# Optimization experiments

Hardware: AMD Instinct MI355X
Metric: run time of the kernel (lower is better)

Reference implementation:

```python
import jax, jax.numpy as jnp
import numpy as np

H = 16      # query heads
KV = 4      # kv heads
HD = 128    # head dim
THETA = 10000.0
NEG = -1e9


def _rope_tables(S, dtype):
    inv_freq = 1.0 / (THETA ** (jnp.arange(0, HD, 2, dtype=jnp.float32) / HD))
    ang = jnp.arange(S, dtype=jnp.float32)[:, None] * inv_freq[None, :]  # [S, HD/2]
    emb = jnp.concatenate([ang, ang], axis=-1)  # [S, HD]
    return jnp.cos(emb).astype(dtype), jnp.sin(emb).astype(dtype)


def _rotate_half(x):
    x1, x2 = jnp.split(x, 2, axis=-1)
    return jnp.concatenate([-x2, x1], axis=-1)


def _apply_rope(t, cos, sin):
    # t: [B, h, S, HD]; cos/sin: [S, HD]
    return t * cos[None, None] + _rotate_half(t) * sin[None, None]


def setup_inputs() -> dict:
    key = jax.random.key(0)
    ks = jax.random.split(key, 5)
    B, S, D = 2, 2048, 2048
    sc = 0.02
    return {
        "x": jax.random.normal(ks[0], (B, S, D), jnp.float32),
        "wq": jax.random.normal(ks[1], (D, D), jnp.float32) * sc,
        "wk": jax.random.normal(ks[2], (KV * HD, D), jnp.float32) * sc,
        "wv": jax.random.normal(ks[3], (KV * HD, D), jnp.float32) * sc,
        "wo": jax.random.normal(ks[4], (D, D), jnp.float32) * sc,
    }


def reference(x, wq, wk, wv, wo):
    B, S, D = x.shape
    q = (x @ wq.T).reshape(B, S, H, HD).transpose(0, 2, 1, 3)   # [B,H,S,HD]
    k = (x @ wk.T).reshape(B, S, KV, HD).transpose(0, 2, 1, 3)  # [B,KV,S,HD]
    v = (x @ wv.T).reshape(B, S, KV, HD).transpose(0, 2, 1, 3)

    cos, sin = _rope_tables(S, x.dtype)
    q = _apply_rope(q, cos, sin)
    k = _apply_rope(k, cos, sin)

    # GQA: repeat kv heads to match query heads (q_group_num = H // KV)
    k = jnp.repeat(k, H // KV, axis=1)  # [B,H,S,HD]
    v = jnp.repeat(v, H // KV, axis=1)

    scores = jnp.einsum("bhqd,bhkd->bhqk", q, k) / jnp.sqrt(jnp.float32(HD)).astype(x.dtype)
    causal = jnp.where(jnp.tril(jnp.ones((S, S), bool)), 0.0, NEG).astype(jnp.float32)
    attn = jax.nn.softmax(scores.astype(jnp.float32) + causal, axis=-1).astype(x.dtype)

    out = jnp.einsum("bhqk,bhkd->bhqd", attn, v)  # [B,H,S,HD]
    out = out.transpose(0, 2, 1, 3).reshape(B, S, D)
    return out @ wo.T
```

## Files before the change

kernel.cpp:

```cpp
#include <hip/hip_runtime.h>
#include <math.h>

typedef unsigned short u16;
typedef __attribute__((ext_vector_type(8))) short short8;
typedef __attribute__((ext_vector_type(8))) __bf16 bf16x8;
typedef __attribute__((ext_vector_type(4))) float floatx4;
typedef __attribute__((ext_vector_type(16))) float floatx16;
typedef __attribute__((ext_vector_type(4))) unsigned short u16x4;
typedef __attribute__((ext_vector_type(4))) float float4v;
typedef __attribute__((ext_vector_type(4))) unsigned int uint4v;

static __device__ __forceinline__ float b2f(u16 u) {
  unsigned int x = ((unsigned int)u) << 16;
  return __builtin_bit_cast(float, x);
}
static __device__ __forceinline__ u16 f2b(float f) {
  unsigned int x = __builtin_bit_cast(unsigned int, f);
  x += 0x7fffu + ((x >> 16) & 1u);
  return (u16)(x >> 16);
}
static __device__ __forceinline__ unsigned int pk2(float lo, float hi) {
  unsigned int r;
  asm("v_cvt_pk_bf16_f32 %0, %1, %2" : "=v"(r) : "v"(lo), "v"(hi));
  return r;
}
static __device__ __forceinline__ void gload_lds16(const void* g, void* l) {
  __builtin_amdgcn_global_load_lds(
      (const __attribute__((address_space(1))) unsigned int*)g,
      (__attribute__((address_space(3))) unsigned int*)l, 16, 0, 0);
}

__global__ __launch_bounds__(256) void cvt5_kernel(
    const float* __restrict__ x, const float* __restrict__ wq,
    const float* __restrict__ wk, const float* __restrict__ wv,
    const float* __restrict__ wo, u16* __restrict__ xb, u16* __restrict__ wqb,
    u16* __restrict__ wkb, u16* __restrict__ wvb, u16* __restrict__ wob) {
  int bid = blockIdx.x;
  const float* in;
  u16* out;
  int i0;
  if (bid < 8192) { in = x; out = xb; i0 = bid; }
  else if (bid < 12288) { in = wq; out = wqb; i0 = bid - 8192; }
  else if (bid < 13312) { in = wk; out = wkb; i0 = bid - 12288; }
  else if (bid < 14336) { in = wv; out = wvb; i0 = bid - 13312; }
  else { in = wo; out = wob; i0 = bid - 14336; }
  int i = i0 * 256 + threadIdx.x;
  float4v v = reinterpret_cast<const float4v*>(in)[i];
  u16x4 o;
  o[0] = f2b(v[0]); o[1] = f2b(v[1]); o[2] = f2b(v[2]); o[3] = f2b(v[3]);
  reinterpret_cast<u16x4*>(out)[i] = o;
}

__global__ __launch_bounds__(256) void rope_table_kernel(float* __restrict__ ct,
                                                         float* __restrict__ st) {
  int idx = blockIdx.x * 256 + threadIdx.x;
  int s = idx >> 6, j = idx & 63;
  float inv = powf(10000.0f, -(float)j * (1.0f / 64.0f));
  float ang = (float)s * inv;
  ct[idx] = cosf(ang);
  st[idx] = sinf(ang);
}

__global__ __launch_bounds__(256) void rope_k_kernel(const u16* __restrict__ in,
                                                     u16* __restrict__ out,
                                                     const float* __restrict__ ct,
                                                     const float* __restrict__ st) {
  int idx = blockIdx.x * 256 + threadIdx.x;
  int jc = idx & 7;
  int rest = idx >> 3;
  int h = rest & 3;
  int bs = rest >> 2;
  int s = bs & 2047;
  int b = bs >> 11;
  int j0 = jc * 8;
  size_t inoff = (size_t)bs * 3072 + 2048 + h * 128 + j0;
  short8 lo = *reinterpret_cast<const short8*>(&in[inoff]);
  short8 hi = *reinterpret_cast<const short8*>(&in[inoff + 64]);
  short8 o0, o1;
#pragma unroll
  for (int e = 0; e < 8; ++e) {
    float c = ct[s * 64 + j0 + e], sn = st[s * 64 + j0 + e];
    float t1 = b2f((u16)lo[e]);
    float t2 = b2f((u16)hi[e]);
    o0[e] = (short)f2b(t1 * c - t2 * sn);
    o1[e] = (short)f2b(t2 * c + t1 * sn);
  }
  size_t ooff = ((size_t)(b * 4 + h) * 2048 + s) * 128 + j0;
  *reinterpret_cast<short8*>(&out[ooff]) = o0;
  *reinterpret_cast<short8*>(&out[ooff + 64]) = o1;
}

__global__ __launch_bounds__(256) void vtrans_kernel(const u16* __restrict__ in,
                                                     u16* __restrict__ out) {
  __shared__ u16 t[128][66];
  int s0 = blockIdx.x * 64;
  int b = blockIdx.y >> 2, kv = blockIdx.y & 3;
  int tid = threadIdx.x;
#pragma unroll
  for (int it = 0; it < 32; ++it) {
    int idx = it * 256 + tid;
    int sl = idx >> 7, d = idx & 127;
    t[d][sl] = in[(size_t)(b * 2048 + s0 + sl) * 3072 + 2560 + kv * 128 + d];
  }
  __syncthreads();
#pragma unroll
  for (int it = 0; it < 32; ++it) {
    int idx = it * 256 + tid;
    int d = idx >> 6, sl = idx & 63;
    out[(size_t)((b * 4 + kv) * 128 + d) * 2048 + s0 + sl] = t[d][sl];
  }
}

static __device__ __forceinline__ void store_out(u16* p, float v) { *p = f2b(v); }
static __device__ __forceinline__ void store_out(float* p, float v) { *p = v; }

template <typename OutT>
__global__ __launch_bounds__(256) void gemm_bt(const u16* __restrict__ A,
                                               const u16* __restrict__ B,
                                               OutT* __restrict__ C, int M, int N, int K) {
  __shared__ __align__(16) u16 Al[128 * 32];
  __shared__ __align__(16) u16 Bl[128 * 32];
  const int tid = threadIdx.x;
  const int lane = tid & 63;
  const int w = tid >> 6;
  const int wr = w >> 1, wc = w & 1;
  const int lr = lane & 15, lg = lane >> 4;
  const int brow = blockIdx.y, bcol = blockIdx.x;
  const int r0 = lane >> 2, kp = lane & 3;
  const u16* Ag = A + (size_t)(brow * 128) * K;
  const u16* Bg = B + (size_t)(bcol * 128) * K;
  floatx4 acc[4][4] = {};
  for (int k0 = 0; k0 < K; k0 += 32) {
#pragma unroll
    for (int j = 0; j < 2; ++j) {
      int c = w * 2 + j;
      int row = c * 16 + r0;
      gload_lds16(Ag + (size_t)row * K + k0 + kp * 8, &Al[c * 512]);
      gload_lds16(Bg + (size_t)row * K + k0 + kp * 8, &Bl[c * 512]);
    }
    __syncthreads();
    bf16x8 af[4], bfr[4];
#pragma unroll
    for (int m = 0; m < 4; ++m)
      af[m] = *reinterpret_cast<const bf16x8*>(&Al[(wr * 64 + m * 16 + lr) * 32 + lg * 8]);
#pragma unroll
    for (int n = 0; n < 4; ++n)
      bfr[n] = *reinterpret_cast<const bf16x8*>(&Bl[(wc * 64 + n * 16 + lr) * 32 + lg * 8]);
#pragma unroll
    for (int m = 0; m < 4; ++m)
#pragma unroll
      for (int n = 0; n < 4; ++n)
        acc[m][n] = __builtin_amdgcn_mfma_f32_16x16x32_bf16(af[m], bfr[n], acc[m][n], 0, 0, 0);
    __syncthreads();
  }
#pragma unroll
  for (int m = 0; m < 4; ++m) {
    int row = brow * 128 + wr * 64 + m * 16 + lg * 4;
#pragma unroll
    for (int n = 0; n < 4; ++n) {
      int col = bcol * 128 + wc * 64 + n * 16 + lr;
#pragma unroll
      for (int i = 0; i < 4; ++i) store_out(&C[(size_t)(row + i) * N + col], acc[m][n][i]);
    }
  }
}

__global__ __launch_bounds__(256, 2) void attn_kernel(
    const u16* __restrict__ QKV, const u16* __restrict__ K,
    const u16* __restrict__ V, const float* __restrict__ ct,
    const float* __restrict__ st, u16* __restrict__ O, u16* __restrict__ Opart,
    float* __restrict__ Mpart, float* __restrict__ Lpart) {
  __shared__ __align__(16) u16 Kl[2][64 * 128];
  __shared__ __align__(16) u16 Vl[2][128 * 64];
  const int tid = threadIdx.x, lane = tid & 63, w = tid >> 6;
  const int ql = lane & 31, h2 = lane >> 5;
  const int idx = blockIdx.x;
  const int bh = idx & 31, pp = (idx >> 5) & 7, half = idx >> 8;
  const int b = bh >> 4, hh = bh & 15, kv = hh >> 2;
  const int t_l = 15 - pp, t_s = pp;
  const int pidx = bh * 8 + pp;
  const u16* Kp = K + (size_t)(b * 4 + kv) * 2048 * 128;
  const u16* Vp = V + (size_t)(b * 4 + kv) * 128 * 2048;
  const float cl = 0.08838834764831845f * 1.44269504088896f;

  auto stage = [&](int buf, int kb) {
#pragma unroll
    for (int j = 0; j < 4; ++j) {
      int slot = j * 256 + tid;
      int row = slot >> 4, d16 = slot & 15;
      gload_lds16(Kp + (size_t)(kb * 64 + row) * 128 + (d16 ^ (row & 15)) * 8,
                  &Kl[buf][(j * 256 + w * 64) * 8]);
      int d = slot >> 3, k8 = slot & 7;
      gload_lds16(Vp + (size_t)d * 2048 + kb * 64 + (k8 ^ (d & 7)) * 8,
                  &Vl[buf][(j * 256 + w * 64) * 8]);
    }
  };

  auto run_segment = [&](int t, int kvs, int kve, int part) {
    const int q0w = t * 128 + w * 32;
    const int qg = q0w + ql;
    bf16x8 qa[8];
    {
      const u16* qp = QKV + ((size_t)(b * 2048 + qg)) * 3072 + hh * 128;
      short8 rr[8];
#pragma unroll
      for (int dk = 0; dk < 8; ++dk)
        rr[dk] = *reinterpret_cast<const short8*>(qp + dk * 16 + h2 * 8);
      const float* cb = ct + (size_t)qg * 64;
      const float* sb = st + (size_t)qg * 64;
#pragma unroll
      for (int dk = 0; dk < 4; ++dk) {
        short8 olo, ohi;
#pragma unroll
        for (int e = 0; e < 8; ++e) {
          int j = dk * 16 + h2 * 8 + e;
          float c = cb[j], sn = sb[j];
          float t1 = b2f((u16)rr[dk][e]);
          float t2 = b2f((u16)rr[dk + 4][e]);
          olo[e] = (short)f2b(t1 * c - t2 * sn);
          ohi[e] = (short)f2b(t2 * c + t1 * sn);
        }
        qa[dk] = __builtin_bit_cast(bf16x8, olo);
        qa[dk + 4] = __builtin_bit_cast(bf16x8, ohi);
      }
    }
    float m_r = -1e30f, l_r = 0.0f;
    floatx16 oacc[4] = {};
    stage(0, kvs);
    __syncthreads();
    int cur = 0;
    for (int kb = kvs; kb < kve; ++kb) {
      if (kb + 1 < kve) stage(cur ^ 1, kb + 1);
      if (kb * 64 <= q0w + 31) {
        const u16* Klc = Kl[cur];
        const u16* Vlc = Vl[cur];
        floatx16 sT0 = {}, sT1 = {};
        __builtin_amdgcn_s_setprio(1);
#pragma unroll
        for (int dk = 0; dk < 8; ++dk) {
          int row0 = ql, row1 = 32 + ql;
          bf16x8 ak0 = *reinterpret_cast<const bf16x8*>(
              &Klc[row0 * 128 + (((dk * 2 + h2) ^ (row0 & 15))) * 8]);
          bf16x8 ak1 = *reinterpret_cast<const bf16x8*>(
              &Klc[row1 * 128 + (((dk * 2 + h2) ^ (row1 & 15))) * 8]);
          sT0 = __builtin_amdgcn_mfma_f32_32x32x16_bf16(ak0, qa[dk], sT0, 0, 0, 0);
          sT1 = __builtin_amdgcn_mfma_f32_32x32x16_bf16(ak1, qa[dk], sT1, 0, 0, 0);
        }
        __builtin_amdgcn_s_setprio(0);
        float x[32];
        const bool domask = (kb * 64 + 63 > q0w);
#pragma unroll
        for (int rg = 0; rg < 16; ++rg) {
          int kloc0 = (rg & 3) + 8 * (rg >> 2) + 4 * h2;
          float v0 = sT0[rg] * cl;
          float v1 = sT1[rg] * cl;
          if (domask) {
            if (kb * 64 + kloc0 > qg) v0 = -1e30f;
            if (kb * 64 + 32 + kloc0 > qg) v1 = -1e30f;
          }
          x[rg] = v0;
          x[16 + rg] = v1;
        }
        float mx[16];
#pragma unroll
        for (int i = 0; i < 16; ++i) mx[i] = fmaxf(x[i], x[i + 16]);
#pragma unroll
        for (int i = 0; i < 8; ++i) mx[i] = fmaxf(mx[i], mx[i + 8]);
#pragma unroll
        for (int i = 0; i < 4; ++i) mx[i] = fmaxf(mx[i], mx[i + 4]);
        float tmax = fmaxf(fmaxf(mx[0], mx[1]), fmaxf(mx[2], mx[3]));
        tmax = fmaxf(tmax, __shfl_xor(tmax, 32));
        if (!__all(tmax - m_r <= 11.0f)) {
          float mn = fmaxf(m_r, tmax);
          float al = exp2f(m_r - mn);
          m_r = mn;
          l_r *= al;
#pragma unroll
          for (int rg = 0; rg < 16; ++rg) {
            int rowq = (rg & 3) + 8 * (rg >> 2) + 4 * h2;
            float arow = __shfl(al, rowq);
            oacc[0][rg] *= arow; oacc[1][rg] *= arow;
            oacc[2][rg] *= arow; oacc[3][rg] *= arow;
          }
        }
        float p[32];
#pragma unroll
        for (int i = 0; i < 32; ++i) p[i] = exp2f(x[i] - m_r);
        float sm[16];
#pragma unroll
        for (int i = 0; i < 16; ++i) sm[i] = p[i] + p[i + 16];
#pragma unroll
        for (int i = 0; i < 8; ++i) sm[i] += sm[i + 8];
#pragma unroll
        for (int i = 0; i < 4; ++i) sm[i] += sm[i + 4];
        float ts = (sm[0] + sm[1]) + (sm[2] + sm[3]);
        ts += __shfl_xor(ts, 32);
        l_r += ts;
        bf16x8 pa[4];
#pragma unroll
        for (int ka = 0; ka < 2; ++ka) {
          const int o = ka * 16;
          unsigned int x0 = pk2(p[o + 0], p[o + 1]);
          unsigned int x1 = pk2(p[o + 2], p[o + 3]);
          unsigned int y0 = pk2(p[o + 4], p[o + 5]);
          unsigned int y1 = pk2(p[o + 6], p[o + 7]);
          asm volatile("v_permlane32_swap_b32 %0, %1" : "+v"(x0), "+v"(y0));
          asm volatile("v_permlane32_swap_b32 %0, %1" : "+v"(x1), "+v"(y1));
          uint4v f0 = {x0, x1, y0, y1};
          pa[ka * 2] = __builtin_bit_cast(bf16x8, f0);
          unsigned int z0 = pk2(p[o + 8], p[o + 9]);
          unsigned int z1 = pk2(p[o + 10], p[o + 11]);
          unsigned int u0 = pk2(p[o + 12], p[o + 13]);
          unsigned int u1 = pk2(p[o + 14], p[o + 15]);
          asm volatile("v_permlane32_swap_b32 %0, %1" : "+v"(z0), "+v"(u0));
          asm volatile("v_permlane32_swap_b32 %0, %1" : "+v"(z1), "+v"(u1));
          uint4v f1 = {z0, z1, u0, u1};
          pa[ka * 2 + 1] = __builtin_bit_cast(bf16x8, f1);
        }
        __builtin_amdgcn_s_setprio(1);
#pragma unroll
        for (int tb = 0; tb < 4; ++tb) {
          int d = tb * 32 + ql;
#pragma unroll
          for (int ks = 0; ks < 4; ++ks) {
            bf16x8 bv = *reinterpret_cast<const bf16x8*>(
                &Vlc[d * 64 + (((ks * 2 + h2) ^ (d & 7))) * 8]);
            oacc[tb] = __builtin_amdgcn_mfma_f32_32x32x16_bf16(pa[ks], bv, oacc[tb], 0, 0, 0);
          }
        }
        __builtin_amdgcn_s_setprio(0);
      }
      __syncthreads();
      cur ^= 1;
    }
    if (part < 0) {
      float linv = 1.0f / l_r;
#pragma unroll
      for (int rg = 0; rg < 16; ++rg) {
        int rowq = (rg & 3) + 8 * (rg >> 2) + 4 * h2;
        float inv = __shfl(linv, rowq);
        int qrow = t * 128 + w * 32 + rowq;
        size_t base = ((size_t)(b * 2048 + qrow)) * 2048 + hh * 128 + ql;
#pragma unroll
        for (int tb = 0; tb < 4; ++tb)
          O[base + tb * 32] = f2b(oacc[tb][rg] * inv);
      }
    } else {
      size_t pb = ((size_t)(part * 256 + pidx)) * 128;
#pragma unroll
      for (int rg = 0; rg < 16; ++rg) {
        int rowq = (rg & 3) + 8 * (rg >> 2) + 4 * h2;
        size_t base = (pb + w * 32 + rowq) * 128 + ql;
#pragma unroll
        for (int tb = 0; tb < 4; ++tb)
          Opart[base + tb * 32] = f2b(oacc[tb][rg]);
      }
      if (h2 == 0) {
        Mpart[pb + w * 32 + ql] = m_r;
        Lpart[pb + w * 32 + ql] = l_r;
      }
    }
  };

  if (half == 0) {
    run_segment(t_l, 0, 17, 0);
  } else {
    run_segment(t_l, 17, 2 * t_l + 2, 1);
    run_segment(t_s, 0, 2 * t_s + 2, -1);
  }
}

__global__ __launch_bounds__(256) void combine_kernel(
    const u16* __restrict__ Opart, const float* __restrict__ Mpart,
    const float* __restrict__ Lpart, u16* __restrict__ O) {
  int pidx = blockIdx.x;
  int bh = pidx >> 3, pp = pidx & 7;
  int b = bh >> 4, hh = bh & 15;
  int t_l = 15 - pp;
  int tid = threadIdx.x;
  int row = tid >> 1, colbase = (tid & 1) * 64;
  size_t pb0 = (size_t)pidx * 128 + row;
  size_t pb1 = (size_t)(256 + pidx) * 128 + row;
  float m0 = Mpart[pb0], m1 = Mpart[pb1];
  float l0 = Lpart[pb0], l1 = Lpart[pb1];
  float M = fmaxf(m0, m1);
  float w0 = exp2f(m0 - M), w1 = exp2f(m1 - M);
  float inv = 1.0f / (w0 * l0 + w1 * l1);
  size_t ob = ((size_t)(b * 2048 + t_l * 128 + row)) * 2048 + hh * 128 + colbase;
#pragma unroll
  for (int k = 0; k < 8; ++k) {
    short8 o0 = *reinterpret_cast<const short8*>(&Opart[pb0 * 128 + colbase + k * 8]);
    short8 o1 = *reinterpret_cast<const short8*>(&Opart[pb1 * 128 + colbase + k * 8]);
    short8 r;
#pragma unroll
    for (int e = 0; e < 8; ++e)
      r[e] = (short)f2b((w0 * b2f((u16)o0[e]) + w1 * b2f((u16)o1[e])) * inv);
    *reinterpret_cast<short8*>(&O[ob + k * 8]) = r;
  }
}

extern "C" void kernel_launch(void* const* d_in, const int* in_sizes, int n_in,
                              void* d_out, int out_size, void* d_ws, size_t ws_size,
                              hipStream_t stream) {
  const float* x  = (const float*)d_in[0];
  const float* wq = (const float*)d_in[1];
  const float* wk = (const float*)d_in[2];
  const float* wv = (const float*)d_in[3];
  const float* wo = (const float*)d_in[4];
  float* out = (float*)d_out;
  char* ws = (char*)d_ws;
  size_t off = 0;
  auto alloc = [&](size_t bytes) -> void* {
    void* p = ws + off;
    off = (off + bytes + 255) & ~(size_t)255;
    return p;
  };
  u16* xb   = (u16*)alloc(4096ull * 2048 * 2);
  u16* wqb  = (u16*)alloc(2048ull * 2048 * 2);
  u16* wkb  = (u16*)alloc(512ull * 2048 * 2);
  u16* wvb  = (u16*)alloc(512ull * 2048 * 2);
  u16* wob  = (u16*)alloc(2048ull * 2048 * 2);
  u16* qkv  = (u16*)alloc(4096ull * 3072 * 2);
  u16* kr   = (u16*)alloc(4096ull * 512 * 2);
  u16* vtb  = (u16*)alloc(4096ull * 512 * 2);
  float* ctab = (float*)alloc(2048ull * 64 * 4);
  float* stab = (float*)alloc(2048ull * 64 * 4);
  u16* opart  = (u16*)alloc(2ull * 256 * 128 * 128 * 2);
  float* mpart = (float*)alloc(2ull * 256 * 128 * 4);
  float* lpart = (float*)alloc(2ull * 256 * 128 * 4);
  u16* attnb = xb;
  (void)in_sizes; (void)n_in; (void)out_size; (void)ws_size;

  cvt5_kernel<<<18432, 256, 0, stream>>>(x, wq, wk, wv, wo, xb, wqb, wkb, wvb, wob);
  rope_table_kernel<<<512, 256, 0, stream>>>(ctab, stab);

  gemm_bt<u16><<<dim3(24, 32), 256, 0, stream>>>(xb, wqb, qkv, 4096, 3072, 2048);

  rope_k_kernel<<<512, 256, 0, stream>>>(qkv, kr, ctab, stab);
  vtrans_kernel<<<dim3(32, 8), 256, 0, stream>>>(qkv, vtb);

  attn_kernel<<<dim3(512), 256, 0, stream>>>(qkv, kr, vtb, ctab, stab, attnb,
                                             opart, mpart, lpart);
  combine_kernel<<<dim3(256), 256, 0, stream>>>(opart, mpart, lpart, attnb);

  gemm_bt<float><<<dim3(16, 32), 256, 0, stream>>>(attnb, wob, out, 4096, 2048, 2048);
}
```

Measured before the change: 235.8 us.

## Triple-buffer GEMM LDS tiles with async prefetch two tiles ahead

```diff
diff --git a/kernel.cpp b/kernel.cpp
--- a/kernel.cpp
+++ b/kernel.cpp
@@ -118,8 +118,8 @@
 __global__ __launch_bounds__(256) void gemm_bt(const u16* __restrict__ A,
                                                const u16* __restrict__ B,
                                                OutT* __restrict__ C, int M, int N, int K) {
-  __shared__ __align__(16) u16 Al[128 * 32];
-  __shared__ __align__(16) u16 Bl[128 * 32];
+  __shared__ __align__(16) u16 Al[3][128 * 32];
+  __shared__ __align__(16) u16 Bl[3][128 * 32];
   const int tid = threadIdx.x;
   const int lane = tid & 63;
   const int w = tid >> 6;
@@ -130,28 +130,46 @@
   const u16* Ag = A + (size_t)(brow * 128) * K;
   const u16* Bg = B + (size_t)(bcol * 128) * K;
   floatx4 acc[4][4] = {};
-  for (int k0 = 0; k0 < K; k0 += 32) {
+  const int NT = K >> 5;
+
+  auto stage = [&](int buf, int t) {
 #pragma unroll
     for (int j = 0; j < 2; ++j) {
       int c = w * 2 + j;
       int row = c * 16 + r0;
-      gload_lds16(Ag + (size_t)row * K + k0 + kp * 8, &Al[c * 512]);
-      gload_lds16(Bg + (size_t)row * K + k0 + kp * 8, &Bl[c * 512]);
-    }
-    __syncthreads();
+      gload_lds16(Ag + (size_t)row * K + t * 32 + kp * 8, &Al[buf][c * 512]);
+      gload_lds16(Bg + (size_t)row * K + t * 32 + kp * 8, &Bl[buf][c * 512]);
+    }
+  };
+
+  stage(0, 0);
+  stage(1, 1);
+  asm volatile("s_waitcnt vmcnt(4)\n\ts_barrier" ::: "memory");
+
+  int cur = 0, nxt = 2;
+  for (int t = 0; t < NT; ++t) {
+    if (t + 2 < NT) stage(nxt, t + 2);
     bf16x8 af[4], bfr[4];
 #pragma unroll
     for (int m = 0; m < 4; ++m)
-      af[m] = *reinterpret_cast<const bf16x8*>(&Al[(wr * 64 + m * 16 + lr) * 32 + lg * 8]);
+      af[m] = *reinterpret_cast<const bf16x8*>(&Al[cur][(wr * 64 + m * 16 + lr) * 32 + lg * 8]);
 #pragma unroll
     for (int n = 0; n < 4; ++n)
-      bfr[n] = *reinterpret_cast<const bf16x8*>(&Bl[(wc * 64 + n * 16 + lr) * 32 + lg * 8]);
+      bfr[n] = *reinterpret_cast<const bf16x8*>(&Bl[cur][(wc * 64 + n * 16 + lr) * 32 + lg * 8]);
+    __builtin_amdgcn_s_setprio(1);
 #pragma unroll
     for (int m = 0; m < 4; ++m)
 #pragma unroll
       for (int n = 0; n < 4; ++n)
         acc[m][n] = __builtin_amdgcn_mfma_f32_16x16x32_bf16(af[m], bfr[n], acc[m][n], 0, 0, 0);
-    __syncthreads();
+    __builtin_amdgcn_s_setprio(0);
+    if (t + 2 < NT) {
+      asm volatile("s_waitcnt vmcnt(4)\n\ts_barrier" ::: "memory");
+    } else if (t + 1 < NT) {
+      asm volatile("s_waitcnt vmcnt(0)\n\ts_barrier" ::: "memory");
+    }
+    cur = (cur == 2) ? 0 : cur + 1;
+    nxt = (nxt == 2) ? 0 : nxt + 1;
   }
 #pragma unroll
   for (int m = 0; m < 4; ++m) {
```

After: 226.7 us. -3.9%, faster.
